# Performance work log

Hardware: AMD Instinct MI355X
Metric: run time of the kernel (lower is better)

## Reference

```python
import jax, jax.numpy as jnp
import numpy as np

ALPHA = 1.0
BETA = 1.0


def setup_inputs() -> dict:
    key = jax.random.key(0)
    k1, k2, k3, k4 = jax.random.split(key, 4)
    B_, S, D_in, D_out, R = 4, 64, 8192, 8192, 16
    x = jax.random.normal(k1, (B_, S, D_in), dtype=jnp.float32)
    original_weight = jax.random.normal(k2, (D_out, D_in), dtype=jnp.float32) * 0.02
    A = jax.random.normal(k3, (D_out, R), dtype=jnp.float32) * 0.02
    Bm = jax.random.normal(k4, (R, D_in), dtype=jnp.float32) * 0.02
    return {"x": x, "original_weight": original_weight, "A": A, "B": Bm}


def reference(x, original_weight, A, B):
    # delta_weight = alpha * (A @ B)  -> [D_out, D_in]
    delta_weight = ALPHA * jnp.matmul(A, B)
    # F.linear(x, W + beta*delta) = x @ (W + beta*delta)^T
    W = original_weight + BETA * delta_weight
    return jnp.einsum("bsd,od->bso", x, W)
```

## Files before the change

kernel.cpp:

```cpp
#include <hip/hip_runtime.h>
#include <stdint.h>


#define DM 256
#define DK 8192
#define DN 8192
#define RLORA 16

#define TN 256
#define BK 64
#define KSPLIT 8
#define KCHUNK (DK / KSPLIT)
#define NITER (KCHUNK / BK)

typedef short bf16x8 __attribute__((ext_vector_type(8)));
typedef float f32x4v __attribute__((ext_vector_type(4)));

typedef __attribute__((address_space(1))) const unsigned char glbc_u8;
typedef __attribute__((address_space(3))) unsigned char lds_u8;

__device__ __forceinline__ unsigned short f2bf(float f) {
  unsigned u = __builtin_bit_cast(unsigned, f);
  u += 0x7FFFu + ((u >> 16) & 1u);
  return (unsigned short)(u >> 16);
}

__device__ __forceinline__ bf16x8 pack8(float4 a, float4 b) {
  bf16x8 r;
  r[0] = (short)f2bf(a.x); r[1] = (short)f2bf(a.y);
  r[2] = (short)f2bf(a.z); r[3] = (short)f2bf(a.w);
  r[4] = (short)f2bf(b.x); r[5] = (short)f2bf(b.y);
  r[6] = (short)f2bf(b.z); r[7] = (short)f2bf(b.w);
  return r;
}

__global__ __launch_bounds__(256) void prep_x(
    const float* __restrict__ x, const float* __restrict__ Bm,
    unsigned short* __restrict__ xb, float* __restrict__ y32) {
  const int ks = blockIdx.x;
  const int m0 = blockIdx.y * 4;
  const int t = threadIdx.x;
  const int k = ks * 1024 + t * 4;
  const int it = (k >> 6) & 15, s = (k >> 5) & 1, oct = (k >> 3) & 3;
  const int e = k & 7;
  float4 xv[4];
#pragma unroll
  for (int i = 0; i < 4; ++i) {
    const int m = m0 + i;
    const int g = m >> 4, r = m & 15;
    xv[i] = *(const float4*)(x + (size_t)m * DK + k);
    ushort4 h;
    h.x = f2bf(xv[i].x); h.y = f2bf(xv[i].y);
    h.z = f2bf(xv[i].z); h.w = f2bf(xv[i].w);
    const size_t chunk = (size_t)((ks * 16 + it) * 32 + s * 16 + g) * 64 + oct * 16 + r;
    *(ushort4*)(xb + chunk * 8 + e) = h;
  }
  float acc[4][RLORA];
#pragma unroll
  for (int r = 0; r < RLORA; ++r) {
    float4 b = *(const float4*)(Bm + (size_t)r * DK + k);
#pragma unroll
    for (int i = 0; i < 4; ++i)
      acc[i][r] = xv[i].x * b.x + xv[i].y * b.y + xv[i].z * b.z + xv[i].w * b.w;
  }
#pragma unroll
  for (int off = 32; off >= 1; off >>= 1)
#pragma unroll
    for (int i = 0; i < 4; ++i)
#pragma unroll
      for (int r = 0; r < RLORA; ++r)
        acc[i][r] += __shfl_xor(acc[i][r], off, 64);
  __shared__ float red[4][4][RLORA];
  const int lane = t & 63, wv = t >> 6;
  if (lane == 0) {
#pragma unroll
    for (int i = 0; i < 4; ++i)
#pragma unroll
      for (int r = 0; r < RLORA; ++r) red[wv][i][r] = acc[i][r];
  }
  __syncthreads();
  if (t < 64) {
    int i = t >> 4, r = t & 15;
    float sum = red[0][i][r] + red[1][i][r] + red[2][i][r] + red[3][i][r];
    atomicAdd(y32 + (m0 + i) * RLORA + r, sum);
  }
}

__global__ __launch_bounds__(256) void pack_y(
    const float* __restrict__ y32, unsigned short* __restrict__ yb) {
  int slot = blockIdx.x * 256 + threadIdx.x;
  int fy = slot >> 6, l = slot & 63;
  int oct = l >> 4, r = l & 15;
  int m = fy * 16 + r;
  unsigned short v[8];
#pragma unroll
  for (int e = 0; e < 8; ++e) {
    int c = oct * 8 + e;
    v[e] = (c < RLORA) ? f2bf(y32[m * RLORA + c]) : (unsigned short)0;
  }
  *(ushort4*)(yb + slot * 8) = make_ushort4(v[0], v[1], v[2], v[3]);
  *(ushort4*)(yb + slot * 8 + 4) = make_ushort4(v[4], v[5], v[6], v[7]);
}

__global__ __launch_bounds__(1024) void lora_gemm(
    const unsigned short* __restrict__ xb,
    const float* __restrict__ W,
    const unsigned short* __restrict__ yb,
    const float* __restrict__ Aw,
    float* __restrict__ out,
    float* __restrict__ part) {
  __shared__ unsigned short xsm[2][16384];
  __shared__ unsigned short wsm[2][16384];

  const int tid = threadIdx.x;
  const int lane = tid & 63, w = tid >> 6;
  const int mi = w >> 2, ni = w & 3;
  const int qr = lane & 15, quad = lane >> 4;
  const int n0 = blockIdx.x * TN;
  const int kz = blockIdx.y;
  const int kb = kz * KCHUNK;

  const int trow = tid >> 2;
  const int tc = (tid & 3) * 16;
  const float* wrow = W + (size_t)(n0 + trow) * DK + kb + tc;
  const int ws_ = tc >> 5, q0 = (tc >> 3) & 3;
  const unsigned wA =
      (unsigned)(((ws_ * 16 + (trow >> 4)) * 64 + q0 * 16 + (trow & 15)) * 16);
  const char* xg = (const char*)xb +
      ((size_t)(kz * 16) * 32 * 64 + (size_t)(w * 2) * 64 + lane) * 16;
  const unsigned xoff = (unsigned)(((w * 2) * 64 + lane) * 16);

  f32x4v acc[4][4];
#pragma unroll
  for (int a = 0; a < 4; ++a)
#pragma unroll
    for (int b = 0; b < 4; ++b) acc[a][b] = (f32x4v){0.f, 0.f, 0.f, 0.f};

  float4 g0 = *(const float4*)(wrow);
  float4 g1 = *(const float4*)(wrow + 4);
  float4 g2 = *(const float4*)(wrow + 8);
  float4 g3 = *(const float4*)(wrow + 12);
  __builtin_amdgcn_global_load_lds((glbc_u8*)xg,
      (lds_u8*)((char*)xsm[0] + xoff), 16, 0, 0);
  __builtin_amdgcn_global_load_lds((glbc_u8*)(xg + 1024),
      (lds_u8*)((char*)xsm[0] + xoff + 1024), 16, 0, 0);
  *(bf16x8*)((char*)wsm[0] + wA) = pack8(g0, g1);
  *(bf16x8*)((char*)wsm[0] + wA + 256) = pack8(g2, g3);
  __syncthreads();

  for (int it = 0; it < NITER; ++it) {
    char* xcur = (char*)xsm[it & 1];
    char* xnxt = (char*)xsm[(it + 1) & 1];
    char* wcur = (char*)wsm[it & 1];
    char* wnxt = (char*)wsm[(it + 1) & 1];
    const bool havW = (it + 1 < NITER);
    if (havW) {
      const float* wsrc = wrow + (size_t)(it + 1) * BK;
      g0 = *(const float4*)(wsrc);
      g1 = *(const float4*)(wsrc + 4);
      g2 = *(const float4*)(wsrc + 8);
      g3 = *(const float4*)(wsrc + 12);
      const char* xs2 = xg + (size_t)(it + 1) * 32768;
      __builtin_amdgcn_global_load_lds((glbc_u8*)xs2,
          (lds_u8*)(xnxt + xoff), 16, 0, 0);
      __builtin_amdgcn_global_load_lds((glbc_u8*)(xs2 + 1024),
          (lds_u8*)(xnxt + xoff + 1024), 16, 0, 0);
    } else if (kz == 0) {
      __builtin_amdgcn_global_load_lds(
          (glbc_u8*)((const char*)yb + (w * 64 + lane) * 16),
          (lds_u8*)(xnxt + (w * 64 + lane) * 16), 16, 0, 0);
    }
#pragma unroll
    for (int s = 0; s < 2; ++s) {
      bf16x8 a[4], b[4];
#pragma unroll
      for (int mt = 0; mt < 4; ++mt)
        a[mt] = *(const bf16x8*)(xcur + (((s * 16 + mi * 4 + mt) * 64 + lane) * 16));
#pragma unroll
      for (int sub = 0; sub < 4; ++sub)
        b[sub] = *(const bf16x8*)(wcur + (((s * 16 + ni * 4 + sub) * 64 + lane) * 16));
#pragma unroll
      for (int mt = 0; mt < 4; ++mt)
#pragma unroll
        for (int sub = 0; sub < 4; ++sub)
          acc[mt][sub] = __builtin_amdgcn_mfma_f32_16x16x32_bf16(
              a[mt], b[sub], acc[mt][sub], 0, 0, 0);
    }
    if (havW) {
      *(bf16x8*)(wnxt + wA) = pack8(g0, g1);
      *(bf16x8*)(wnxt + wA + 256) = pack8(g2, g3);
    }
    __syncthreads();
  }

  if (kz == 0) {
    const char* ybase = (const char*)xsm[0];
    bf16x8 b[4];
    float4 z = {0.f, 0.f, 0.f, 0.f};
#pragma unroll
    for (int sub = 0; sub < 4; ++sub) {
      int n_l = ni * 64 + sub * 16 + qr;
      const float* ap = Aw + (size_t)(n0 + n_l) * RLORA + quad * 8;
      float4 p0 = (quad < 2) ? *(const float4*)(ap) : z;
      float4 p1 = (quad < 2) ? *(const float4*)(ap + 4) : z;
      b[sub] = pack8(p0, p1);
    }
#pragma unroll
    for (int mt = 0; mt < 4; ++mt) {
      bf16x8 av = *(const bf16x8*)(ybase + (((mi * 4 + mt) * 64 + lane) * 16));
#pragma unroll
      for (int sub = 0; sub < 4; ++sub)
        acc[mt][sub] = __builtin_amdgcn_mfma_f32_16x16x32_bf16(
            av, b[sub], acc[mt][sub], 0, 0, 0);
    }
  }

  if (part) {
    float* pb = part + (size_t)kz * DM * DN;
#pragma unroll
    for (int mt = 0; mt < 4; ++mt)
#pragma unroll
      for (int sub = 0; sub < 4; ++sub) {
        float* p = pb + (size_t)(mi * 64 + mt * 16 + quad * 4) * DN +
                   n0 + ni * 64 + sub * 16 + qr;
#pragma unroll
        for (int rg = 0; rg < 4; ++rg) p[(size_t)rg * DN] = acc[mt][sub][rg];
      }
  } else {
    float* ob = out;
#pragma unroll
    for (int mt = 0; mt < 4; ++mt)
#pragma unroll
      for (int sub = 0; sub < 4; ++sub) {
        float* p = ob + (size_t)(mi * 64 + mt * 16 + quad * 4) * DN +
                   n0 + ni * 64 + sub * 16 + qr;
#pragma unroll
        for (int rg = 0; rg < 4; ++rg) atomicAdd(p + (size_t)rg * DN, acc[mt][sub][rg]);
      }
  }
}

__global__ __launch_bounds__(256) void reduce_k(
    const float* __restrict__ part, float* __restrict__ out) {
  size_t i = ((size_t)blockIdx.x * 256 + threadIdx.x) * 4;
  float4 s = *(const float4*)(part + i);
#pragma unroll
  for (int kzi = 1; kzi < KSPLIT; ++kzi) {
    float4 v = *(const float4*)(part + (size_t)kzi * DM * DN + i);
    s.x += v.x; s.y += v.y; s.z += v.z; s.w += v.w;
  }
  *(float4*)(out + i) = s;
}

extern "C" void kernel_launch(void* const* d_in, const int* in_sizes, int n_in,
                              void* d_out, int out_size, void* d_ws, size_t ws_size,
                              hipStream_t stream) {
  const float* x  = (const float*)d_in[0];
  const float* W  = (const float*)d_in[1];
  const float* A  = (const float*)d_in[2];
  const float* Bm = (const float*)d_in[3];
  float* out = (float*)d_out;

  unsigned short* xb = (unsigned short*)d_ws;
  unsigned short* yb = (unsigned short*)((char*)d_ws + (4u << 20));
  float* y32 = (float*)((char*)yb + 16384);
  size_t base_bytes = (4u << 20) + 16384 + 16384;
  size_t part_bytes = (size_t)KSPLIT * DM * DN * 4;
  bool use_part = ws_size >= base_bytes + part_bytes;
  float* part = use_part ? (float*)((char*)d_ws + base_bytes) : nullptr;

  if (!use_part)
    hipMemsetAsync(d_out, 0, (size_t)out_size * sizeof(float), stream);
  hipMemsetAsync(y32, 0, (size_t)DM * RLORA * sizeof(float), stream);
  prep_x<<<dim3(8, 64), 256, 0, stream>>>(x, Bm, xb, y32);
  pack_y<<<4, 256, 0, stream>>>(y32, yb);
  lora_gemm<<<dim3(DN / TN, KSPLIT), 1024, 0, stream>>>(xb, W, yb, A, out, part);
  if (use_part) reduce_k<<<2048, 256, 0, stream>>>(part, out);
}
```

Before: 452.6 us.

## Shrink GEMM N-tile, read bf16 x fragments directly from global, halve K-split

The main GEMM now uses 64-wide N tiles with 512-thread blocks and a K-split of 4 instead of 256-wide tiles, 1024 threads and a K-split of 8. The x operand is no longer staged in LDS through global_load_lds; each wave loads its bf16 fragments straight from global memory, which is expected to hit in L2. Only the W tile is double-buffered in a much smaller LDS buffer, which lets more blocks share a CU and halves the partial-sum traffic. The trade-off is more redundant global and L2 reads of x across the larger number of N blocks, and less reuse of x per block.

```diff
diff --git a/kernel.cpp b/kernel.cpp
--- a/kernel.cpp
+++ b/kernel.cpp
@@ -7,17 +7,14 @@
 #define DN 8192
 #define RLORA 16
 
-#define TN 256
+#define TN 64
 #define BK 64
-#define KSPLIT 8
+#define KSPLIT 4
 #define KCHUNK (DK / KSPLIT)
 #define NITER (KCHUNK / BK)
 
 typedef short bf16x8 __attribute__((ext_vector_type(8)));
 typedef float f32x4v __attribute__((ext_vector_type(4)));
-
-typedef __attribute__((address_space(1))) const unsigned char glbc_u8;
-typedef __attribute__((address_space(3))) unsigned char lds_u8;
 
 __device__ __forceinline__ unsigned short f2bf(float f) {
   unsigned u = __builtin_bit_cast(unsigned, f);
@@ -41,7 +38,7 @@
   const int m0 = blockIdx.y * 4;
   const int t = threadIdx.x;
   const int k = ks * 1024 + t * 4;
-  const int it = (k >> 6) & 15, s = (k >> 5) & 1, oct = (k >> 3) & 3;
+  const int K64 = k >> 6, s = (k >> 5) & 1, oct = (k >> 3) & 3;
   const int e = k & 7;
   float4 xv[4];
 #pragma unroll
@@ -52,7 +49,7 @@
     ushort4 h;
     h.x = f2bf(xv[i].x); h.y = f2bf(xv[i].y);
     h.z = f2bf(xv[i].z); h.w = f2bf(xv[i].w);
-    const size_t chunk = (size_t)((ks * 16 + it) * 32 + s * 16 + g) * 64 + oct * 16 + r;
+    const size_t chunk = (size_t)(K64 * 32 + s * 16 + g) * 64 + oct * 16 + r;
     *(ushort4*)(xb + chunk * 8 + e) = h;
   }
   float acc[4][RLORA];
@@ -102,114 +99,92 @@
   *(ushort4*)(yb + slot * 8 + 4) = make_ushort4(v[4], v[5], v[6], v[7]);
 }
 
-__global__ __launch_bounds__(1024) void lora_gemm(
+__global__ __launch_bounds__(512, 4) void lora_gemm(
     const unsigned short* __restrict__ xb,
     const float* __restrict__ W,
     const unsigned short* __restrict__ yb,
     const float* __restrict__ Aw,
     float* __restrict__ out,
     float* __restrict__ part) {
-  __shared__ unsigned short xsm[2][16384];
-  __shared__ unsigned short wsm[2][16384];
+  __shared__ unsigned short wsm[2][4096];
 
   const int tid = threadIdx.x;
   const int lane = tid & 63, w = tid >> 6;
-  const int mi = w >> 2, ni = w & 3;
+  const int mi = w >> 1, ni = w & 1;
   const int qr = lane & 15, quad = lane >> 4;
   const int n0 = blockIdx.x * TN;
   const int kz = blockIdx.y;
   const int kb = kz * KCHUNK;
 
-  const int trow = tid >> 2;
-  const int tc = (tid & 3) * 16;
-  const float* wrow = W + (size_t)(n0 + trow) * DK + kb + tc;
-  const int ws_ = tc >> 5, q0 = (tc >> 3) & 3;
-  const unsigned wA =
-      (unsigned)(((ws_ * 16 + (trow >> 4)) * 64 + q0 * 16 + (trow & 15)) * 16);
-  const char* xg = (const char*)xb +
-      ((size_t)(kz * 16) * 32 * 64 + (size_t)(w * 2) * 64 + lane) * 16;
-  const unsigned xoff = (unsigned)(((w * 2) * 64 + lane) * 16);
-
-  f32x4v acc[4][4];
+  const int Fs = w >> 2, Fsub = w & 3;
+  const float* wsrc = W + (size_t)(n0 + Fsub * 16 + qr) * DK + kb +
+                      Fs * 32 + quad * 8;
+  const unsigned wdst = (unsigned)tid * 16;
+
+  const bf16x8* ap = (const bf16x8*)xb + ((size_t)(kz * 32) * 32) * 64 + lane;
+
+  f32x4v acc[4][2];
 #pragma unroll
   for (int a = 0; a < 4; ++a)
 #pragma unroll
-    for (int b = 0; b < 4; ++b) acc[a][b] = (f32x4v){0.f, 0.f, 0.f, 0.f};
-
-  float4 g0 = *(const float4*)(wrow);
-  float4 g1 = *(const float4*)(wrow + 4);
-  float4 g2 = *(const float4*)(wrow + 8);
-  float4 g3 = *(const float4*)(wrow + 12);
-  __builtin_amdgcn_global_load_lds((glbc_u8*)xg,
-      (lds_u8*)((char*)xsm[0] + xoff), 16, 0, 0);
-  __builtin_amdgcn_global_load_lds((glbc_u8*)(xg + 1024),
-      (lds_u8*)((char*)xsm[0] + xoff + 1024), 16, 0, 0);
-  *(bf16x8*)((char*)wsm[0] + wA) = pack8(g0, g1);
-  *(bf16x8*)((char*)wsm[0] + wA + 256) = pack8(g2, g3);
+    for (int b = 0; b < 2; ++b) acc[a][b] = (f32x4v){0.f, 0.f, 0.f, 0.f};
+
+  float4 g0 = *(const float4*)(wsrc);
+  float4 g1 = *(const float4*)(wsrc + 4);
+  *(bf16x8*)((char*)wsm[0] + wdst) = pack8(g0, g1);
   __syncthreads();
 
   for (int it = 0; it < NITER; ++it) {
-    char* xcur = (char*)xsm[it & 1];
-    char* xnxt = (char*)xsm[(it + 1) & 1];
-    char* wcur = (char*)wsm[it & 1];
+    const char* wcur = (const char*)wsm[it & 1];
     char* wnxt = (char*)wsm[(it + 1) & 1];
     const bool havW = (it + 1 < NITER);
     if (havW) {
-      const float* wsrc = wrow + (size_t)(it + 1) * BK;
-      g0 = *(const float4*)(wsrc);
-      g1 = *(const float4*)(wsrc + 4);
-      g2 = *(const float4*)(wsrc + 8);
-      g3 = *(const float4*)(wsrc + 12);
-      const char* xs2 = xg + (size_t)(it + 1) * 32768;
-      __builtin_amdgcn_global_load_lds((glbc_u8*)xs2,
-          (lds_u8*)(xnxt + xoff), 16, 0, 0);
-      __builtin_amdgcn_global_load_lds((glbc_u8*)(xs2 + 1024),
-          (lds_u8*)(xnxt + xoff + 1024), 16, 0, 0);
-    } else if (kz == 0) {
-      __builtin_amdgcn_global_load_lds(
-          (glbc_u8*)((const char*)yb + (w * 64 + lane) * 16),
-          (lds_u8*)(xnxt + (w * 64 + lane) * 16), 16, 0, 0);
-    }
+      const float* p = wsrc + (size_t)(it + 1) * BK;
+      g0 = *(const float4*)(p);
+      g1 = *(const float4*)(p + 4);
+    }
+    bf16x8 av[4][2];
+#pragma unroll
+    for (int s = 0; s < 2; ++s)
+#pragma unroll
+      for (int mt = 0; mt < 4; ++mt)
+        av[mt][s] = ap[(size_t)(s * 16 + mi * 4 + mt) * 64];
+    ap += (size_t)32 * 64;
 #pragma unroll
     for (int s = 0; s < 2; ++s) {
-      bf16x8 a[4], b[4];
+      bf16x8 b[2];
+#pragma unroll
+      for (int sub = 0; sub < 2; ++sub)
+        b[sub] = *(const bf16x8*)(wcur +
+            (((s * 4 + ni * 2 + sub) * 64 + lane) * 16));
 #pragma unroll
       for (int mt = 0; mt < 4; ++mt)
-        a[mt] = *(const bf16x8*)(xcur + (((s * 16 + mi * 4 + mt) * 64 + lane) * 16));
-#pragma unroll
-      for (int sub = 0; sub < 4; ++sub)
-        b[sub] = *(const bf16x8*)(wcur + (((s * 16 + ni * 4 + sub) * 64 + lane) * 16));
-#pragma unroll
-      for (int mt = 0; mt < 4; ++mt)
-#pragma unroll
-        for (int sub = 0; sub < 4; ++sub)
+#pragma unroll
+        for (int sub = 0; sub < 2; ++sub)
           acc[mt][sub] = __builtin_amdgcn_mfma_f32_16x16x32_bf16(
-              a[mt], b[sub], acc[mt][sub], 0, 0, 0);
-    }
-    if (havW) {
-      *(bf16x8*)(wnxt + wA) = pack8(g0, g1);
-      *(bf16x8*)(wnxt + wA + 256) = pack8(g2, g3);
-    }
+              av[mt][s], b[sub], acc[mt][sub], 0, 0, 0);
+    }
+    if (havW) *(bf16x8*)(wnxt + wdst) = pack8(g0, g1);
     __syncthreads();
   }
 
   if (kz == 0) {
-    const char* ybase = (const char*)xsm[0];
-    bf16x8 b[4];
     float4 z = {0.f, 0.f, 0.f, 0.f};
-#pragma unroll
-    for (int sub = 0; sub < 4; ++sub) {
-      int n_l = ni * 64 + sub * 16 + qr;
-      const float* ap = Aw + (size_t)(n0 + n_l) * RLORA + quad * 8;
-      float4 p0 = (quad < 2) ? *(const float4*)(ap) : z;
-      float4 p1 = (quad < 2) ? *(const float4*)(ap + 4) : z;
+    bf16x8 b[2];
+#pragma unroll
+    for (int sub = 0; sub < 2; ++sub) {
+      const float* ap2 = Aw + (size_t)(n0 + ni * 32 + sub * 16 + qr) * RLORA +
+                         quad * 8;
+      float4 p0 = (quad < 2) ? *(const float4*)(ap2) : z;
+      float4 p1 = (quad < 2) ? *(const float4*)(ap2 + 4) : z;
       b[sub] = pack8(p0, p1);
     }
+    const bf16x8* yp = (const bf16x8*)yb + lane;
 #pragma unroll
     for (int mt = 0; mt < 4; ++mt) {
-      bf16x8 av = *(const bf16x8*)(ybase + (((mi * 4 + mt) * 64 + lane) * 16));
-#pragma unroll
-      for (int sub = 0; sub < 4; ++sub)
+      bf16x8 av = yp[(size_t)(mi * 4 + mt) * 64];
+#pragma unroll
+      for (int sub = 0; sub < 2; ++sub)
         acc[mt][sub] = __builtin_amdgcn_mfma_f32_16x16x32_bf16(
             av, b[sub], acc[mt][sub], 0, 0, 0);
     }
@@ -220,9 +195,9 @@
 #pragma unroll
     for (int mt = 0; mt < 4; ++mt)
 #pragma unroll
-      for (int sub = 0; sub < 4; ++sub) {
+      for (int sub = 0; sub < 2; ++sub) {
         float* p = pb + (size_t)(mi * 64 + mt * 16 + quad * 4) * DN +
-                   n0 + ni * 64 + sub * 16 + qr;
+                   n0 + ni * 32 + sub * 16 + qr;
 #pragma unroll
         for (int rg = 0; rg < 4; ++rg) p[(size_t)rg * DN] = acc[mt][sub][rg];
       }
@@ -231,11 +206,12 @@
 #pragma unroll
     for (int mt = 0; mt < 4; ++mt)
 #pragma unroll
-      for (int sub = 0; sub < 4; ++sub) {
+      for (int sub = 0; sub < 2; ++sub) {
         float* p = ob + (size_t)(mi * 64 + mt * 16 + quad * 4) * DN +
-                   n0 + ni * 64 + sub * 16 + qr;
-#pragma unroll
-        for (int rg = 0; rg < 4; ++rg) atomicAdd(p + (size_t)rg * DN, acc[mt][sub][rg]);
+                   n0 + ni * 32 + sub * 16 + qr;
+#pragma unroll
+        for (int rg = 0; rg < 4; ++rg)
+          atomicAdd(p + (size_t)rg * DN, acc[mt][sub][rg]);
       }
   }
 }
@@ -274,6 +250,6 @@
   hipMemsetAsync(y32, 0, (size_t)DM * RLORA * sizeof(float), stream);
   prep_x<<<dim3(8, 64), 256, 0, stream>>>(x, Bm, xb, y32);
   pack_y<<<4, 256, 0, stream>>>(y32, yb);
-  lora_gemm<<<dim3(DN / TN, KSPLIT), 1024, 0, stream>>>(xb, W, yb, A, out, part);
+  lora_gemm<<<dim3(DN / TN, KSPLIT), 512, 0, stream>>>(xb, W, yb, A, out, part);
   if (use_part) reduce_k<<<2048, 256, 0, stream>>>(part, out);
 }
```

New measurement: 443.7 us. 2.0% less time.
